# Kernel tuning notes

Hardware: AMD Instinct MI355X
Metric: run time of the kernel (lower is better)

The kernel has to match this reference:

```python
import jax, jax.numpy as jnp
import numpy as np

COL = 14
NJ = 14
SIGMA = 1.0
RADIUS = 4  # int(truncate*sigma + 0.5) with scipy defaults truncate=4.0
B = 8192
C = NJ + 4  # 14 joint channels + 4 group channels


def _gauss_kernel():
    x = np.arange(-RADIUS, RADIUS + 1).astype(np.float32)
    k = np.exp(-0.5 * x * x / (SIGMA * SIGMA))
    return jnp.asarray(k / k.sum(), jnp.float32)


def _gaussian_filter(x):
    # x: [N, H, W]; scipy gaussian_filter(sigma=1.0, mode='reflect') == symmetric pad + separable conv
    k = _gauss_kernel()
    xp = jnp.pad(x, ((0, 0), (RADIUS, RADIUS), (RADIUS, RADIUS)), mode='symmetric')
    y = jax.lax.conv_general_dilated(xp[:, None, :, :], k.reshape(1, 1, 2 * RADIUS + 1, 1), (1, 1), 'VALID')
    y = jax.lax.conv_general_dilated(y, k.reshape(1, 1, 1, 2 * RADIUS + 1), (1, 1), 'VALID')
    return y[:, 0]


def setup_inputs() -> dict:
    key = jax.random.key(0)
    k1, k2, k3, k4 = jax.random.split(key, 4)
    return {
        'os': jax.random.normal(k1, (B, 2 * NJ, COL, COL), dtype=jnp.float32),
        'h': jax.random.normal(k2, (B, C, COL, COL), dtype=jnp.float32),
        't': jax.random.uniform(k3, (B, NJ, 2), dtype=jnp.float32),
        'v': jax.random.randint(k4, (B, NJ, 2), 0, 2, dtype=jnp.int32),
    }


def reference(os, h, t, v):
    b = h.shape[0]
    # pixel indices: int() truncation then clamp to [0, 13]
    ti = jax.lax.stop_gradient(t) * COL
    idx = jnp.clip(ti.astype(jnp.int32), 0, COL - 1)
    xi, yi = idx[..., 0], idx[..., 1]
    vis = (v[..., 0] == 1)  # [B, NJ]

    ar = jnp.arange(COL)
    onehot = ((ar[:, None] == yi[..., None, None]) & (ar[None, :] == xi[..., None, None])).astype(h.dtype)  # [B,NJ,14,14]
    joint_hot = onehot * vis[..., None, None].astype(h.dtype)

    # 4 group channels from joints 0:3, 3:6, 6:9, 9:12 (set to 1, i.e. max, not add)
    ghot = joint_hot[:, :12].reshape(b, 4, 3, COL, COL).max(axis=2)
    gvis = vis[:, :12].reshape(b, 4, 3).any(axis=2)

    hot = jnp.concatenate([joint_hot, ghot], axis=1)        # [B, 18, 14, 14]
    mask = jnp.concatenate([vis, gvis], axis=1)             # [B, 18]

    filt = _gaussian_filter(hot.reshape(b * C, COL, COL)).reshape(b, C, COL, COL)
    mn = filt.min(axis=(-2, -1), keepdims=True)
    mx = filt.max(axis=(-2, -1), keepdims=True)
    denom = jnp.where(mx - mn == 0, jnp.ones_like(mx), mx - mn)
    tt = jnp.where(mask[..., None, None], (filt - mn) / denom, jnp.zeros_like(filt))

    diff = (h - tt) * mask[..., None, None].astype(h.dtype)
    n1 = v.sum().astype(h.dtype) / 2
    return jnp.sum(diff * diff) / n1
```

## Files before the change

kernel.cpp:

```cpp
#include <hip/hip_runtime.h>

#define NB   8192
#define NJ   14
#define NC   18
#define PIX  196
#define CHE  (NC * PIX)
#define BPB  4
#define NBLK (NB / BPB)
#define GSTR 16
#define ZROW 14

#define WSUM_INV 0.398943491f

__global__ __launch_bounds__(256, 8) void mse_partial_kernel(
    const float* __restrict__ h, const float* __restrict__ t,
    const int* __restrict__ v, float2* __restrict__ partials)
{
    __shared__ float  gs[15 * GSTR];
    __shared__ float  gmn[14], gmx[14];
    __shared__ float  st[BPB * 28];
    __shared__ int    sv[BPB * 28];
    __shared__ float4 list[BPB * NC];
    __shared__ float  wvs[BPB];
    __shared__ float  wred[BPB];

    const int tid = threadIdx.x;
    const int b0  = blockIdx.x * BPB;
    const int w   = tid >> 6, lane = tid & 63;

    if (tid < BPB * 28)               st[tid] = t[b0 * 28 + tid];
    else if (tid < 2 * BPB * 28)      sv[tid - BPB * 28] = v[b0 * 28 + (tid - BPB * 28)];
    if (tid < 15 * GSTR) {
        int p = tid >> 4, r = tid & 15;
        float val = 0.f;
        if (p < 14 && r < 14) {
            const float wl[9] = {0.00033546262f, 0.011108997f, 0.13533528f, 0.60653066f,
                                 1.0f, 0.60653066f, 0.13533528f, 0.011108997f, 0.00033546262f};
            float acc = 0.f;
            #pragma unroll
            for (int k = 0; k < 9; k++) {
                int m  = r + k - 4;
                int sm = m < 0 ? (-m - 1) : (m > 13 ? 27 - m : m);
                if (sm == p) acc += wl[k];
            }
            val = acc * WSUM_INV;
        }
        gs[tid] = val;
    }
    __syncthreads();

    if (tid < 14) {
        float mn = 1e30f, mx = -1e30f;
        #pragma unroll
        for (int r = 0; r < 14; r++) { float x = gs[tid * GSTR + r]; mn = fminf(mn, x); mx = fmaxf(mx, x); }
        gmn[tid] = mn; gmx[tid] = mx;
    }
    __syncthreads();

    int rb_[4], cb_[4], vld_[4];
    #pragma unroll
    for (int q = 0; q < 4; q++) {
        int e = lane + 64 * q;
        vld_[q] = (e < PIX);
        int ee = vld_[q] ? e : PIX - 1;
        int rr = ee / 14, cc = ee - 14 * rr;
        rb_[q] = rr << 2; cb_[q] = cc << 2;
    }

    int xi = 0, yi = 0, vis = 0;
    if (lane < NJ) {
        float fx = st[w * 28 + 2 * lane];
        float fy = st[w * 28 + 2 * lane + 1];
        xi = (int)(fx * 14.0f); xi = xi < 0 ? 0 : (xi > 13 ? 13 : xi);
        yi = (int)(fy * 14.0f); yi = yi < 0 ? 0 : (yi > 13 ? 13 : yi);
        vis = (sv[w * 28 + 2 * lane] == 1);
    }
    const int code = (vis << 8) | (xi << 4) | yi;

    float nmn_c = 0.f, inv_c = 0.f;
    int   pos_c = 0, act_c = 0, np_c = 0;
    if (lane < NJ && vis) {
        float mn = gmn[yi] * gmn[xi], mx = gmx[yi] * gmx[xi];
        float den = mx - mn; if (den == 0.f) den = 1.f;
        inv_c = 1.f / den; nmn_c = -mn * inv_c; act_c = 1; np_c = 1;
        pos_c = yi | (xi << 4);
    }
    for (int gi = 0; gi < 4; gi++) {
        int c0  = __shfl(code, 3 * gi);
        int c1_ = __shfl(code, 3 * gi + 1);
        int c2  = __shfl(code, 3 * gi + 2);
        int packed = 0, np = 0;
        if (c0 & 0x100) { packed = c0 & 0xFF; np = 1; }
        if (c1_ & 0x100) {
            int pc = c1_ & 0xFF;
            bool dup = (np > 0) && ((packed & 0xFF) == pc);
            if (!dup) { packed |= pc << (8 * np); np++; }
        }
        if (c2 & 0x100) {
            int pc = c2 & 0xFF;
            bool dup = false;
            for (int s = 0; s < np; s++) if (((packed >> (8 * s)) & 0xFF) == pc) dup = true;
            if (!dup) { packed |= pc << (8 * np); np++; }
        }
        int pp = packed;
        if (np < 2) pp |= ZROW << 8;
        if (np < 3) pp |= ZROW << 16;

        float mn = 0.f, mx = 0.f;
        if (np == 1) {
            int y = packed & 15, x = (packed >> 4) & 15;
            mn = gmn[y] * gmn[x]; mx = gmx[y] * gmx[x];
        } else if (np >= 2) {
            const int spp = __builtin_amdgcn_readfirstlane(pp);
            const int o0 = ( spp        & 15) << 6, p0 = ((spp >> 4)  & 15) << 6;
            const int o1 = ((spp >> 8)  & 15) << 6, p1 = ((spp >> 12) & 15) << 6;
            const int o2 = ((spp >> 16) & 15) << 6, p2 = ((spp >> 20) & 15) << 6;
            const char* g8 = (const char*)gs;
            float lmn = 1e30f, lmx = -1e30f;
            #pragma unroll
            for (int q2 = 0; q2 < 4; q2++) {
                float f = *(const float*)(g8 + o0 + rb_[q2]) * *(const float*)(g8 + p0 + cb_[q2])
                        + *(const float*)(g8 + o1 + rb_[q2]) * *(const float*)(g8 + p1 + cb_[q2])
                        + *(const float*)(g8 + o2 + rb_[q2]) * *(const float*)(g8 + p2 + cb_[q2]);
                lmn = fminf(lmn, vld_[q2] ? f : 1e30f);
                lmx = fmaxf(lmx, vld_[q2] ? f : -1e30f);
            }
            #pragma unroll
            for (int m = 1; m < 64; m <<= 1) {
                lmn = fminf(lmn, __shfl_xor(lmn, m));
                lmx = fmaxf(lmx, __shfl_xor(lmx, m));
            }
            mn = lmn; mx = lmx;
        }
        if (lane == NJ + gi && np > 0) {
            float den = mx - mn; if (den == 0.f) den = 1.f;
            inv_c = 1.f / den; nmn_c = -mn * inv_c; act_c = 1; np_c = np;
            pos_c = (np == 1) ? (packed & 0xFF) : pp;
        }
    }
    {
        int vval = (lane < 28) ? sv[w * 28 + lane] : 0;
        unsigned long long bal = __ballot(vval == 1);
        if (lane == 0) wvs[w] = (float)__popcll(bal);
    }
    unsigned long long b1 = __ballot(act_c && np_c == 1);
    unsigned long long bX = __ballot(act_c && np_c >= 2);
    const int c1 = __popcll(b1);
    const int cX = __popcll(bX);
    unsigned long long below = (1ull << lane) - 1ull;
    if (act_c) {
        int idx = (np_c == 1) ? __popcll(b1 & below) : c1 + __popcll(bX & below);
        float4 e;
        e.x = nmn_c; e.y = inv_c;
        e.z = __int_as_float(pos_c);
        e.w = __int_as_float(lane * (PIX * 4));
        list[w * NC + idx] = e;
    }

    const char* hb   = (const char*)(h + (size_t)(b0 + w) * CHE);
    const int  lane49 = lane < 48 ? lane : 48;
    const bool lv     = (lane < 49);
    const int  pix0   = lane49 * 4;
    const int  rr0    = pix0 / 14;
    const int  cc0    = pix0 - 14 * rr0;
    const bool wrap   = (cc0 == 12);
    const int  ccB    = wrap ? 0 : cc0 + 2;
    const int  voff   = lane49 * 16;
    const int  brr  = rr0 << 2, bcc = cc0 << 2, bccB = ccB << 2;
    const int  lbase  = w * NC;
    const char* g8 = (const char*)gs;
    float acc = 0.f;

    for (int base = 0; base < c1; base += 4) {
        float nmn[4], inv[4];
        int   syo[4], sxo[4], ok[4];
        float4 hv[4];
        #pragma unroll
        for (int u = 0; u < 4; u++) {
            int ee = base + u;
            ok[u] = (ee < c1);
            ee = ok[u] ? ee : c1 - 1;
            float4 mv = list[lbase + ee];
            nmn[u] = mv.x; inv[u] = mv.y;
            int sp = __builtin_amdgcn_readfirstlane(__float_as_int(mv.z));
            syo[u] = ( sp       & 15) << 6;
            sxo[u] = ((sp >> 4) & 15) << 6;
            int sb = __builtin_amdgcn_readfirstlane(__float_as_int(mv.w));
            hv[u] = *(const float4*)(hb + sb + voff);
        }
        #pragma unroll
        for (int u = 0; u < 4; u++) {
            const float* ry  = (const float*)(g8 + syo[u] + brr);
            const float* rxa = (const float*)(g8 + sxo[u] + bcc);
            const float* rxb = (const float*)(g8 + sxo[u] + bccB);
            float wy0  = ry[0],  wy1  = ry[1];
            float wxA0 = rxa[0], wxA1 = rxa[1];
            float wxB0 = rxb[0], wxB1 = rxb[1];
            float wyC  = wrap ? wy1 : wy0;
            float d0 = hv[u].x - fmaf(wy0 * wxA0, inv[u], nmn[u]);
            float d1 = hv[u].y - fmaf(wy0 * wxA1, inv[u], nmn[u]);
            float d2 = hv[u].z - fmaf(wyC * wxB0, inv[u], nmn[u]);
            float d3 = hv[u].w - fmaf(wyC * wxB1, inv[u], nmn[u]);
            float s  = fmaf(d0, d0, fmaf(d1, d1, fmaf(d2, d2, d3 * d3)));
            acc += (ok[u] && lv) ? s : 0.f;
        }
    }

    const int cT = c1 + cX;
    for (int base = c1; base < cT; base += 2) {
        float nmn[2], inv[2];
        int   sqo[2][6], ok[2];
        float4 hv[2];
        #pragma unroll
        for (int u = 0; u < 2; u++) {
            int ee = base + u;
            ok[u] = (ee < cT);
            ee = ok[u] ? ee : cT - 1;
            float4 mv = list[lbase + ee];
            nmn[u] = mv.x; inv[u] = mv.y;
            int sp = __builtin_amdgcn_readfirstlane(__float_as_int(mv.z));
            #pragma unroll
            for (int q = 0; q < 3; q++) {
                sqo[u][2*q]   = ((sp >> (8*q))     & 15) << 6;
                sqo[u][2*q+1] = ((sp >> (8*q + 4)) & 15) << 6;
            }
            int sb = __builtin_amdgcn_readfirstlane(__float_as_int(mv.w));
            hv[u] = *(const float4*)(hb + sb + voff);
        }
        #pragma unroll
        for (int u = 0; u < 2; u++) {
            float f0 = 0.f, f1 = 0.f, f2 = 0.f, f3 = 0.f;
            #pragma unroll
            for (int q = 0; q < 3; q++) {
                const float* ry  = (const float*)(g8 + sqo[u][2*q]   + brr);
                const float* rxa = (const float*)(g8 + sqo[u][2*q+1] + bcc);
                const float* rxb = (const float*)(g8 + sqo[u][2*q+1] + bccB);
                float wy0  = ry[0],  wy1  = ry[1];
                float wxA0 = rxa[0], wxA1 = rxa[1];
                float wxB0 = rxb[0], wxB1 = rxb[1];
                float wyC  = wrap ? wy1 : wy0;
                f0 = fmaf(wy0, wxA0, f0);
                f1 = fmaf(wy0, wxA1, f1);
                f2 = fmaf(wyC, wxB0, f2);
                f3 = fmaf(wyC, wxB1, f3);
            }
            float d0 = hv[u].x - fmaf(f0, inv[u], nmn[u]);
            float d1 = hv[u].y - fmaf(f1, inv[u], nmn[u]);
            float d2 = hv[u].z - fmaf(f2, inv[u], nmn[u]);
            float d3 = hv[u].w - fmaf(f3, inv[u], nmn[u]);
            float s  = fmaf(d0, d0, fmaf(d1, d1, fmaf(d2, d2, d3 * d3)));
            acc += (ok[u] && lv) ? s : 0.f;
        }
    }

    #pragma unroll
    for (int off = 32; off > 0; off >>= 1) acc += __shfl_down(acc, off);
    if (lane == 0) wred[w] = acc;
    __syncthreads();
    if (tid == 0) {
        float2 pr;
        pr.x = wred[0] + wred[1] + wred[2] + wred[3];
        pr.y = wvs[0] + wvs[1] + wvs[2] + wvs[3];
        partials[blockIdx.x] = pr;
    }
}

__global__ __launch_bounds__(1024) void finalize_kernel(
    const float4* __restrict__ partials4, float* __restrict__ out)
{
    __shared__ float w1[16], w2[16];
    int tid = threadIdx.x;
    float4 p = partials4[tid];
    float s = p.x + p.z, vs = p.y + p.w;
    #pragma unroll
    for (int off = 32; off > 0; off >>= 1) {
        s  += __shfl_down(s, off);
        vs += __shfl_down(vs, off);
    }
    if ((tid & 63) == 0) { w1[tid >> 6] = s; w2[tid >> 6] = vs; }
    __syncthreads();
    if (tid == 0) {
        float stot = 0.f, vtot = 0.f;
        #pragma unroll
        for (int q = 0; q < 16; q++) { stot += w1[q]; vtot += w2[q]; }
        out[0] = stot / (vtot * 0.5f);
    }
}

extern "C" void kernel_launch(void* const* d_in, const int* in_sizes, int n_in,
                              void* d_out, int out_size, void* d_ws, size_t ws_size,
                              hipStream_t stream) {
    const float* h = (const float*)d_in[1];
    const float* t = (const float*)d_in[2];
    const int*   v = (const int*)d_in[3];
    float2* partials = (float2*)d_ws;

    mse_partial_kernel<<<NBLK, 256, 0, stream>>>(h, t, v, partials);
    finalize_kernel<<<1, 1024, 0, stream>>>((const float4*)partials, (float*)d_out);
}
```

Baseline: 23.61 us.

## Double batch per block, load t/v per wave directly, simplify loop tails

Block size grows to 512 threads with 8 batch items per block, halving the block count and amortizing the per-block Gaussian table setup. Each wave now loads its own t and v entries as float2/int2 directly instead of staging them through shared memory, shares joint codes via LDS instead of shuffles, and counts visibility from both v components. The single-joint loop is split into a full-unrolled body plus a masked tail. The multi-joint loop is processed one entry at a time, and the inverse scale is folded into the y-weight to save a multiply. Larger blocks may reduce occupancy flexibility.

```diff
diff --git a/kernel.cpp b/kernel.cpp
--- a/kernel.cpp
+++ b/kernel.cpp
@@ -5,21 +5,20 @@
 #define NC   18
 #define PIX  196
 #define CHE  (NC * PIX)
-#define BPB  4
+#define BPB  8
 #define NBLK (NB / BPB)
 #define GSTR 16
 #define ZROW 14
 
 #define WSUM_INV 0.398943491f
 
-__global__ __launch_bounds__(256, 8) void mse_partial_kernel(
+__global__ __launch_bounds__(512, 8) void mse_partial_kernel(
     const float* __restrict__ h, const float* __restrict__ t,
     const int* __restrict__ v, float2* __restrict__ partials)
 {
     __shared__ float  gs[15 * GSTR];
     __shared__ float  gmn[14], gmx[14];
-    __shared__ float  st[BPB * 28];
-    __shared__ int    sv[BPB * 28];
+    __shared__ int    scode[BPB * 16];
     __shared__ float4 list[BPB * NC];
     __shared__ float  wvs[BPB];
     __shared__ float  wred[BPB];
@@ -27,9 +26,8 @@
     const int tid = threadIdx.x;
     const int b0  = blockIdx.x * BPB;
     const int w   = tid >> 6, lane = tid & 63;
-
-    if (tid < BPB * 28)               st[tid] = t[b0 * 28 + tid];
-    else if (tid < 2 * BPB * 28)      sv[tid - BPB * 28] = v[b0 * 28 + (tid - BPB * 28)];
+    const int b   = b0 + w;
+
     if (tid < 15 * GSTR) {
         int p = tid >> 4, r = tid & 15;
         float val = 0.f;
@@ -48,7 +46,6 @@
         gs[tid] = val;
     }
     __syncthreads();
-
     if (tid < 14) {
         float mn = 1e30f, mx = -1e30f;
         #pragma unroll
@@ -67,15 +64,20 @@
         rb_[q] = rr << 2; cb_[q] = cc << 2;
     }
 
-    int xi = 0, yi = 0, vis = 0;
+    int xi = 0, yi = 0, vis = 0, vy = 0;
     if (lane < NJ) {
-        float fx = st[w * 28 + 2 * lane];
-        float fy = st[w * 28 + 2 * lane + 1];
-        xi = (int)(fx * 14.0f); xi = xi < 0 ? 0 : (xi > 13 ? 13 : xi);
-        yi = (int)(fy * 14.0f); yi = yi < 0 ? 0 : (yi > 13 ? 13 : yi);
-        vis = (sv[w * 28 + 2 * lane] == 1);
-    }
-    const int code = (vis << 8) | (xi << 4) | yi;
+        float2 tv = ((const float2*)t)[b * NJ + lane];
+        int2   vv = ((const int2*)v)[b * NJ + lane];
+        xi = (int)(tv.x * 14.0f); xi = xi < 0 ? 0 : (xi > 13 ? 13 : xi);
+        yi = (int)(tv.y * 14.0f); yi = yi < 0 ? 0 : (yi > 13 ? 13 : yi);
+        vis = (vv.x == 1); vy = (vv.y == 1);
+    }
+    if (lane < NJ) scode[w * 16 + lane] = (vis << 8) | (xi << 4) | yi;
+    {
+        unsigned long long bx = __ballot(lane < NJ && vis);
+        unsigned long long by = __ballot(lane < NJ && vy);
+        if (lane == 0) wvs[w] = (float)(__popcll(bx) + __popcll(by));
+    }
 
     float nmn_c = 0.f, inv_c = 0.f;
     int   pos_c = 0, act_c = 0, np_c = 0;
@@ -86,9 +88,9 @@
         pos_c = yi | (xi << 4);
     }
     for (int gi = 0; gi < 4; gi++) {
-        int c0  = __shfl(code, 3 * gi);
-        int c1_ = __shfl(code, 3 * gi + 1);
-        int c2  = __shfl(code, 3 * gi + 2);
+        int c0  = scode[w * 16 + 3 * gi];
+        int c1_ = scode[w * 16 + 3 * gi + 1];
+        int c2  = scode[w * 16 + 3 * gi + 2];
         int packed = 0, np = 0;
         if (c0 & 0x100) { packed = c0 & 0xFF; np = 1; }
         if (c1_ & 0x100) {
@@ -138,15 +140,10 @@
             pos_c = (np == 1) ? (packed & 0xFF) : pp;
         }
     }
-    {
-        int vval = (lane < 28) ? sv[w * 28 + lane] : 0;
-        unsigned long long bal = __ballot(vval == 1);
-        if (lane == 0) wvs[w] = (float)__popcll(bal);
-    }
     unsigned long long b1 = __ballot(act_c && np_c == 1);
     unsigned long long bX = __ballot(act_c && np_c >= 2);
     const int c1 = __popcll(b1);
-    const int cX = __popcll(bX);
+    const int cT = c1 + __popcll(bX);
     unsigned long long below = (1ull << lane) - 1ull;
     if (act_c) {
         int idx = (np_c == 1) ? __popcll(b1 & below) : c1 + __popcll(bX & below);
@@ -157,7 +154,7 @@
         list[w * NC + idx] = e;
     }
 
-    const char* hb   = (const char*)(h + (size_t)(b0 + w) * CHE);
+    const char* hb   = (const char*)(h + (size_t)b * CHE);
     const int  lane49 = lane < 48 ? lane : 48;
     const bool lv     = (lane < 49);
     const int  pix0   = lane49 * 4;
@@ -166,21 +163,19 @@
     const bool wrap   = (cc0 == 12);
     const int  ccB    = wrap ? 0 : cc0 + 2;
     const int  voff   = lane49 * 16;
-    const int  brr  = rr0 << 2, bcc = cc0 << 2, bccB = ccB << 2;
+    const int  brr = rr0 << 2, bcc = cc0 << 2, bccB = ccB << 2;
     const int  lbase  = w * NC;
     const char* g8 = (const char*)gs;
     float acc = 0.f;
 
-    for (int base = 0; base < c1; base += 4) {
+    const int nfull = c1 & ~3;
+    for (int base = 0; base < nfull; base += 4) {
         float nmn[4], inv[4];
-        int   syo[4], sxo[4], ok[4];
+        int   syo[4], sxo[4];
         float4 hv[4];
         #pragma unroll
         for (int u = 0; u < 4; u++) {
-            int ee = base + u;
-            ok[u] = (ee < c1);
-            ee = ok[u] ? ee : c1 - 1;
-            float4 mv = list[lbase + ee];
+            float4 mv = list[lbase + base + u];
             nmn[u] = mv.x; inv[u] = mv.y;
             int sp = __builtin_amdgcn_readfirstlane(__float_as_int(mv.z));
             syo[u] = ( sp       & 15) << 6;
@@ -196,62 +191,81 @@
             float wy0  = ry[0],  wy1  = ry[1];
             float wxA0 = rxa[0], wxA1 = rxa[1];
             float wxB0 = rxb[0], wxB1 = rxb[1];
-            float wyC  = wrap ? wy1 : wy0;
-            float d0 = hv[u].x - fmaf(wy0 * wxA0, inv[u], nmn[u]);
-            float d1 = hv[u].y - fmaf(wy0 * wxA1, inv[u], nmn[u]);
-            float d2 = hv[u].z - fmaf(wyC * wxB0, inv[u], nmn[u]);
-            float d3 = hv[u].w - fmaf(wyC * wxB1, inv[u], nmn[u]);
-            float s  = fmaf(d0, d0, fmaf(d1, d1, fmaf(d2, d2, d3 * d3)));
-            acc += (ok[u] && lv) ? s : 0.f;
-        }
-    }
-
-    const int cT = c1 + cX;
-    for (int base = c1; base < cT; base += 2) {
-        float nmn[2], inv[2];
-        int   sqo[2][6], ok[2];
-        float4 hv[2];
-        #pragma unroll
-        for (int u = 0; u < 2; u++) {
-            int ee = base + u;
-            ok[u] = (ee < cT);
-            ee = ok[u] ? ee : cT - 1;
-            float4 mv = list[lbase + ee];
+            float wy0i = wy0 * inv[u];
+            float wyCi = (wrap ? wy1 : wy0) * inv[u];
+            float d0 = hv[u].x - fmaf(wy0i, wxA0, nmn[u]);
+            float d1 = hv[u].y - fmaf(wy0i, wxA1, nmn[u]);
+            float d2 = hv[u].z - fmaf(wyCi, wxB0, nmn[u]);
+            float d3 = hv[u].w - fmaf(wyCi, wxB1, nmn[u]);
+            acc += fmaf(d0, d0, fmaf(d1, d1, fmaf(d2, d2, d3 * d3)));
+        }
+    }
+    if (c1 & 3) {
+        float nmn[4], inv[4];
+        int   syo[4], sxo[4], ok[4];
+        float4 hv[4];
+        #pragma unroll
+        for (int u = 0; u < 4; u++) {
+            int ee = nfull + u;
+            ok[u] = (ee < c1);
+            float4 mv = list[lbase + (ok[u] ? ee : c1 - 1)];
             nmn[u] = mv.x; inv[u] = mv.y;
             int sp = __builtin_amdgcn_readfirstlane(__float_as_int(mv.z));
-            #pragma unroll
-            for (int q = 0; q < 3; q++) {
-                sqo[u][2*q]   = ((sp >> (8*q))     & 15) << 6;
-                sqo[u][2*q+1] = ((sp >> (8*q + 4)) & 15) << 6;
-            }
+            syo[u] = ( sp       & 15) << 6;
+            sxo[u] = ((sp >> 4) & 15) << 6;
             int sb = __builtin_amdgcn_readfirstlane(__float_as_int(mv.w));
             hv[u] = *(const float4*)(hb + sb + voff);
         }
         #pragma unroll
-        for (int u = 0; u < 2; u++) {
-            float f0 = 0.f, f1 = 0.f, f2 = 0.f, f3 = 0.f;
-            #pragma unroll
-            for (int q = 0; q < 3; q++) {
-                const float* ry  = (const float*)(g8 + sqo[u][2*q]   + brr);
-                const float* rxa = (const float*)(g8 + sqo[u][2*q+1] + bcc);
-                const float* rxb = (const float*)(g8 + sqo[u][2*q+1] + bccB);
-                float wy0  = ry[0],  wy1  = ry[1];
-                float wxA0 = rxa[0], wxA1 = rxa[1];
-                float wxB0 = rxb[0], wxB1 = rxb[1];
-                float wyC  = wrap ? wy1 : wy0;
-                f0 = fmaf(wy0, wxA0, f0);
-                f1 = fmaf(wy0, wxA1, f1);
-                f2 = fmaf(wyC, wxB0, f2);
-                f3 = fmaf(wyC, wxB1, f3);
-            }
-            float d0 = hv[u].x - fmaf(f0, inv[u], nmn[u]);
-            float d1 = hv[u].y - fmaf(f1, inv[u], nmn[u]);
-            float d2 = hv[u].z - fmaf(f2, inv[u], nmn[u]);
-            float d3 = hv[u].w - fmaf(f3, inv[u], nmn[u]);
+        for (int u = 0; u < 4; u++) {
+            const float* ry  = (const float*)(g8 + syo[u] + brr);
+            const float* rxa = (const float*)(g8 + sxo[u] + bcc);
+            const float* rxb = (const float*)(g8 + sxo[u] + bccB);
+            float wy0  = ry[0],  wy1  = ry[1];
+            float wxA0 = rxa[0], wxA1 = rxa[1];
+            float wxB0 = rxb[0], wxB1 = rxb[1];
+            float wy0i = wy0 * inv[u];
+            float wyCi = (wrap ? wy1 : wy0) * inv[u];
+            float d0 = hv[u].x - fmaf(wy0i, wxA0, nmn[u]);
+            float d1 = hv[u].y - fmaf(wy0i, wxA1, nmn[u]);
+            float d2 = hv[u].z - fmaf(wyCi, wxB0, nmn[u]);
+            float d3 = hv[u].w - fmaf(wyCi, wxB1, nmn[u]);
             float s  = fmaf(d0, d0, fmaf(d1, d1, fmaf(d2, d2, d3 * d3)));
-            acc += (ok[u] && lv) ? s : 0.f;
-        }
-    }
+            acc += ok[u] ? s : 0.f;
+        }
+    }
+
+    for (int e = c1; e < cT; e++) {
+        float4 mv = list[lbase + e];
+        float nmn = mv.x, inv = mv.y;
+        int sp = __builtin_amdgcn_readfirstlane(__float_as_int(mv.z));
+        int sb = __builtin_amdgcn_readfirstlane(__float_as_int(mv.w));
+        float4 hv = *(const float4*)(hb + sb + voff);
+        float f0 = 0.f, f1 = 0.f, f2 = 0.f, f3 = 0.f;
+        #pragma unroll
+        for (int q = 0; q < 3; q++) {
+            int yo = ((sp >> (8 * q))     & 15) << 6;
+            int xo = ((sp >> (8 * q + 4)) & 15) << 6;
+            const float* ry  = (const float*)(g8 + yo + brr);
+            const float* rxa = (const float*)(g8 + xo + bcc);
+            const float* rxb = (const float*)(g8 + xo + bccB);
+            float wy0  = ry[0],  wy1  = ry[1];
+            float wxA0 = rxa[0], wxA1 = rxa[1];
+            float wxB0 = rxb[0], wxB1 = rxb[1];
+            float wyC  = wrap ? wy1 : wy0;
+            f0 = fmaf(wy0, wxA0, f0);
+            f1 = fmaf(wy0, wxA1, f1);
+            f2 = fmaf(wyC, wxB0, f2);
+            f3 = fmaf(wyC, wxB1, f3);
+        }
+        float d0 = hv.x - fmaf(f0, inv, nmn);
+        float d1 = hv.y - fmaf(f1, inv, nmn);
+        float d2 = hv.z - fmaf(f2, inv, nmn);
+        float d3 = hv.w - fmaf(f3, inv, nmn);
+        acc += fmaf(d0, d0, fmaf(d1, d1, fmaf(d2, d2, d3 * d3)));
+    }
+
+    acc = lv ? acc : 0.f;
 
     #pragma unroll
     for (int off = 32; off > 0; off >>= 1) acc += __shfl_down(acc, off);
@@ -259,16 +273,18 @@
     __syncthreads();
     if (tid == 0) {
         float2 pr;
-        pr.x = wred[0] + wred[1] + wred[2] + wred[3];
-        pr.y = wvs[0] + wvs[1] + wvs[2] + wvs[3];
+        float s = 0.f, vs = 0.f;
+        #pragma unroll
+        for (int q = 0; q < BPB; q++) { s += wred[q]; vs += wvs[q]; }
+        pr.x = s; pr.y = vs;
         partials[blockIdx.x] = pr;
     }
 }
 
-__global__ __launch_bounds__(1024) void finalize_kernel(
+__global__ __launch_bounds__(512) void finalize_kernel(
     const float4* __restrict__ partials4, float* __restrict__ out)
 {
-    __shared__ float w1[16], w2[16];
+    __shared__ float w1[8], w2[8];
     int tid = threadIdx.x;
     float4 p = partials4[tid];
     float s = p.x + p.z, vs = p.y + p.w;
@@ -282,7 +298,7 @@
     if (tid == 0) {
         float stot = 0.f, vtot = 0.f;
         #pragma unroll
-        for (int q = 0; q < 16; q++) { stot += w1[q]; vtot += w2[q]; }
+        for (int q = 0; q < 8; q++) { stot += w1[q]; vtot += w2[q]; }
         out[0] = stot / (vtot * 0.5f);
     }
 }
@@ -295,6 +311,6 @@
     const int*   v = (const int*)d_in[3];
     float2* partials = (float2*)d_ws;
 
-    mse_partial_kernel<<<NBLK, 256, 0, stream>>>(h, t, v, partials);
-    finalize_kernel<<<1, 1024, 0, stream>>>((const float4*)partials, (float*)d_out);
+    mse_partial_kernel<<<NBLK, 512, 0, stream>>>(h, t, v, partials);
+    finalize_kernel<<<1, 512, 0, stream>>>((const float4*)partials, (float*)d_out);
 }
```

After: 22.11 us. 1.07x faster.
